# Kernel tuning notes

Hardware: AMD Instinct MI355X
Metric: run time of the kernel (lower is better)

## Reference

```python
import jax, jax.numpy as jnp
import numpy as np

KLD_SCALE = 10.0
COMMIT_COST = 0.25


def setup_inputs() -> dict:
    key = jax.random.key(0)
    k1, k2, k3, k4 = jax.random.split(key, 4)
    B, C, T = 32, 512, 4096
    D, K = 128, 1024
    z = jax.random.normal(k1, (B, C, T), dtype=jnp.float32)
    proj_w = jax.random.normal(k2, (D, C), dtype=jnp.float32) * (1.0 / np.sqrt(C))
    proj_b = jax.random.normal(k3, (D,), dtype=jnp.float32) * 0.01
    embed_w = jax.random.normal(k4, (K, D), dtype=jnp.float32)
    return {"z": z, "proj_w": proj_w, "proj_b": proj_b, "embed_w": embed_w}


def reference(z, proj_w, proj_b, embed_w):
    B, C, T = z.shape
    D = proj_w.shape[0]
    # 1x1 Conv1d == per-timestep linear: [B,C,T] x [D,C] -> [B,T,D]
    z_e = jnp.einsum('bct,dc->btd', z, proj_w) + proj_b
    flat = z_e.reshape(-1, D)  # [B*T, D]
    # squared euclidean distances to codebook: [B*T, K]
    dist = (jnp.sum(flat * flat, axis=1, keepdims=True)
            - 2.0 * (flat @ embed_w.T)
            + jnp.sum(embed_w * embed_w, axis=1)[None, :])
    ind = jnp.argmin(dist, axis=1).reshape(B, T)  # == argmax(-dist)
    z_q = embed_w[ind]  # [B,T,D] codebook gather
    sg = jax.lax.stop_gradient
    diff = KLD_SCALE * (COMMIT_COST * jnp.mean((sg(z_q) - z_e) ** 2)
                        + jnp.mean((z_q - sg(z_e)) ** 2))
    z_q_ste = z_e + sg(z_q - z_e)  # straight-through estimator
    z_q_out = jnp.transpose(z_q_ste, (0, 2, 1))  # [B,D,T]
    return z_q_out, diff, ind
```

## Files before the change

kernel.cpp:

```cpp
#include <hip/hip_runtime.h>

#define B_N 32
#define C_N 512
#define T_N 4096
#define D_N 128
#define K_N 1024
#define N_N (B_N * T_N)

typedef _Float16 f16x8 __attribute__((ext_vector_type(8)));
typedef float    f32x4 __attribute__((ext_vector_type(4)));

#define ZSWZ_OFF 0
#define ESWZ_OFF 67108864
#define ENS_OFF  67895296
#define WSWZ_OFF 68431872
#define PART_OFF 68694016

#define GLL(g, s) __builtin_amdgcn_global_load_lds( \
    (const __attribute__((address_space(1))) unsigned int*)(g), \
    (__attribute__((address_space(3))) unsigned int*)(s), 16, 0, 0)

__global__ __launch_bounds__(128) void k_eprep(const float* __restrict__ E,
                                               _Float16* __restrict__ eswz,
                                               float* __restrict__ ens) {
  __shared__ float s2[2];
  const int code = blockIdx.x, d = threadIdx.x;
  const float e  = E[(size_t)code * D_N + d];
  const float es = e * 64.f;
  const _Float16 eh = (_Float16)es;
  const _Float16 el = (_Float16)(es - (float)eh);

  float sq = es * es;
  #pragma unroll
  for (int off = 32; off > 0; off >>= 1) sq += __shfl_down(sq, off);
  if ((d & 63) == 0) s2[d >> 6] = sq;
  __syncthreads();
  if (d == 0) ens[code] = s2[0] + s2[1];

  const int kt = code >> 7, mi = (code >> 4) & 7, lrow = code & 15;
  const int lk = (d >> 3) & 3, i = d & 7, cb = d >> 5;
  const size_t tile = (size_t)kt * 12;
  #define PUT(c, v) eswz[(((tile + (c)) * 512 + mi * 64 + lk * 16 + lrow) << 3) + i] = (v)
  PUT(cb, eh);
  PUT(4 + cb, el);
  PUT(8 + cb, eh);
  #undef PUT
}

__global__ __launch_bounds__(256) void k_wprep(const float* __restrict__ W,
                                               _Float16* __restrict__ wswz) {
  const int e = blockIdx.x * 256 + threadIdx.x;
  const int d = e >> 9, c = e & 511;
  const float x = W[d * C_N + c] * 8.f;
  const _Float16 h  = (_Float16)x;
  const _Float16 lo = (_Float16)(x - (float)h);
  const int kc = c >> 5, gg = (c >> 3) & 3, j = c & 7;
  const int nf = d >> 4, ll = gg * 16 + (d & 15);
  const size_t base = (size_t)kc * 8192 + ((size_t)nf * 64 + ll) * 8 + j;
  wswz[base]        = h;
  wswz[base + 4096] = lo;
}

__global__ __launch_bounds__(256, 2) void k_projm(const float* __restrict__ z,
                                                  const _Float16* __restrict__ wswz,
                                                  const float* __restrict__ bias,
                                                  f16x8* __restrict__ zswz) {
  __shared__ __align__(16) char lds[65536];

  const int tid = threadIdx.x;
  const int l   = tid & 63, w = tid >> 6;
  const int g   = l >> 4, li = l & 15;
  const int b   = blockIdx.y, t0 = blockIdx.x * 128;
  const float* zb = z + (size_t)b * C_N * T_N + t0;

  float bs[8];
  #pragma unroll
  for (int nf = 0; nf < 8; ++nf) bs[nf] = bias[nf * 16 + li] * 64.f;

  f32x4 acc[2][8];
  #pragma unroll
  for (int mi = 0; mi < 2; ++mi)
    #pragma unroll
    for (int nf = 0; nf < 8; ++nf) acc[mi][nf] = (f32x4)0.f;

  auto stage = [&](int kc, int buf) {
    char* zdst = lds + buf * 16384;
    char* wdst = lds + 32768 + buf * 16384;
    #pragma unroll
    for (int s = 0; s < 4; ++s) {
      const int q = w * 4 + s;
      const unsigned v = q * 64 + l;
      const unsigned u = v ^ (((v >> 8) & 1) << 2);
      GLL((const char*)zb +
              ((size_t)(kc * 32 + (u >> 5)) * T_N + (size_t)(u & 31) * 4) * 4,
          zdst + q * 1024);
      GLL((const char*)wswz + (size_t)kc * 16384 + q * 1024 + l * 16,
          wdst + q * 1024);
    }
  };

  stage(0, 0);
  __syncthreads();

  int buf = 0;
  for (int kc = 0; kc < 16; ++kc) {
    if (kc + 1 < 16) stage(kc + 1, buf ^ 1);

    const float* zl = (const float*)(lds + buf * 16384);
    const f16x8* wb = (const f16x8*)(lds + 32768 + buf * 16384);

    f16x8 ah[2], al[2];
    #pragma unroll
    for (int mi = 0; mi < 2; ++mi) {
      const int mt = w * 2 + mi;
      const int a0 = (g * 1024 + mt * 16 + li) ^ ((g & 1) << 4);
      #pragma unroll
      for (int j = 0; j < 8; ++j) {
        const float x = zl[a0 + j * 128] * 8.f;
        const _Float16 h = (_Float16)x;
        ah[mi][j] = h;
        al[mi][j] = (_Float16)(x - (float)h);
      }
    }
    f16x8 bh[8], bl[8];
    #pragma unroll
    for (int nf = 0; nf < 8; ++nf) {
      bh[nf] = wb[nf * 64 + l];
      bl[nf] = wb[512 + nf * 64 + l];
    }
    #pragma unroll
    for (int mi = 0; mi < 2; ++mi)
      #pragma unroll
      for (int nf = 0; nf < 8; ++nf) {
        acc[mi][nf] = __builtin_amdgcn_mfma_f32_16x16x32_f16(ah[mi], bh[nf], acc[mi][nf], 0, 0, 0);
        acc[mi][nf] = __builtin_amdgcn_mfma_f32_16x16x32_f16(al[mi], bh[nf], acc[mi][nf], 0, 0, 0);
        acc[mi][nf] = __builtin_amdgcn_mfma_f32_16x16x32_f16(ah[mi], bl[nf], acc[mi][nf], 0, 0, 0);
      }
    __syncthreads();
    buf ^= 1;
  }

  unsigned* cs = (unsigned*)lds;
  const int n0 = b * T_N + t0;
  for (int p = 0; p < 2; ++p) {
    #pragma unroll
    for (int mi = 0; mi < 2; ++mi) {
      const int trow = (w * 2 + mi) * 16 + g * 4;
      #pragma unroll
      for (int nfl = 0; nfl < 4; ++nfl) {
        const int nf = p * 4 + nfl;
        #pragma unroll
        for (int r = 0; r < 4; ++r) {
          const float x = acc[mi][nf][r] + bs[nf];
          const _Float16 h  = (_Float16)x;
          const _Float16 lo = (_Float16)(x - (float)h);
          cs[(trow + r) * 68 + nfl * 16 + li] =
              (unsigned)__builtin_bit_cast(unsigned short, h) |
              ((unsigned)__builtin_bit_cast(unsigned short, lo) << 16);
        }
      }
    }
    __syncthreads();
    #pragma unroll
    for (int i = 0; i < 4; ++i) {
      const int u = i * 256 + tid;
      const int t = u & 127, dc = u >> 7;
      f16x8 vh, vl;
      #pragma unroll
      for (int e = 0; e < 8; ++e) {
        const unsigned vv = cs[t * 68 + dc * 8 + e];
        vh[e] = __builtin_bit_cast(_Float16, (unsigned short)(vv & 0xffff));
        vl[e] = __builtin_bit_cast(_Float16, (unsigned short)(vv >> 16));
      }
      const int n = n0 + t;
      const int cu = p * 2 + (dc >> 2), lk = dc & 3;
      const size_t idx = ((size_t)(n >> 4) * 8 + cu) * 64 + lk * 16 + (n & 15);
      zswz[idx]       = vh;
      zswz[idx + 256] = vl;
    }
    __syncthreads();
  }
}

template<int NF0>
__device__ __forceinline__ float gather_lds(int wc, int l, const int* skf,
                                            const float* E, float* ob,
                                            const f16x8* rows) {
  float psum = 0.f;
  #pragma unroll
  for (int nl = 0; nl < 2; ++nl) {
    const int nf = NF0 + nl;
    const int r = wc * 64 + nf * 16 + (l & 15);
    const int k = skf[r];
    const float* Er = E + (size_t)k * D_N;
    #pragma unroll
    for (int cu = 0; cu < 4; ++cu) {
      const int d0 = cu * 32 + (l >> 4) * 8;
      const float4 e0 = *(const float4*)(Er + d0);
      const float4 e1 = *(const float4*)(Er + d0 + 4);
      const float ev[8] = {e0.x, e0.y, e0.z, e0.w, e1.x, e1.y, e1.z, e1.w};
      const f16x8 hi = rows[(((wc * 4 + nf) * 8 + cu) * 64) + l];
      const f16x8 lo = rows[(((wc * 4 + nf) * 8 + cu + 4) * 64) + l];
      #pragma unroll
      for (int j = 0; j < 8; ++j) {
        const float ze = ((float)hi[j] + (float)lo[j]) * 0.015625f;
        const float df = ev[j] - ze;
        psum += df * df;
        ob[(size_t)(d0 + j) * T_N + r] = ev[j];
      }
    }
  }
  return psum;
}

__global__ __launch_bounds__(256, 2) void k_argmin3(const f16x8* __restrict__ zswz,
                                                    const f16x8* __restrict__ eswz,
                                                    const float* __restrict__ ens,
                                                    const float* __restrict__ E,
                                                    float* __restrict__ out,
                                                    float* __restrict__ indf,
                                                    float* __restrict__ part) {
  __shared__ f16x8 rows[4096];
  __shared__ f16x8 abuf[2][512];

  const int tid = threadIdx.x;
  const int l   = tid & 63, w = tid >> 6;
  const int wr  = w >> 1, wc = w & 1;
  const int blk = blockIdx.x;

  const char* zsrc = (const char*)zswz + (size_t)blk * 65536;
  #pragma unroll
  for (int s = 0; s < 16; ++s)
    GLL(zsrc + s * 4096 + tid * 16, &rows[s * 256 + w * 64]);

  {
    const char* asrc = (const char*)eswz;
    GLL(asrc + tid * 16,        &abuf[0][w * 64]);
    GLL(asrc + 4096 + tid * 16, &abuf[0][256 + w * 64]);
  }
  __syncthreads();

  f16x8 bfr[8][4];
  #pragma unroll
  for (int cu = 0; cu < 8; ++cu)
    #pragma unroll
    for (int nf = 0; nf < 4; ++nf)
      bfr[cu][nf] = rows[((wc * 4 + nf) * 8 + cu) * 64 + l];

  float bestd[4];
  int   bestk[4];
  #pragma unroll
  for (int nf = 0; nf < 4; ++nf) { bestd[nf] = 3.4e38f; bestk[nf] = 0; }

  int buf = 0;
  for (int kt = 0; kt < 8; ++kt) {
    f32x4 acc[4][4];
    #pragma unroll
    for (int mi = 0; mi < 4; ++mi)
      #pragma unroll
      for (int nf = 0; nf < 4; ++nf) acc[mi][nf] = (f32x4)0.f;

    #pragma unroll
    for (int c = 0; c < 12; ++c) {
      int nkt = kt, nc = c + 1;
      if (nc == 12) { nc = 0; ++nkt; }
      if (nkt < 8) {
        const char* asrc = (const char*)eswz + ((size_t)(nkt * 12 + nc) * 512) * 16;
        GLL(asrc + tid * 16,        &abuf[buf ^ 1][w * 64]);
        GLL(asrc + 4096 + tid * 16, &abuf[buf ^ 1][256 + w * 64]);
      }
      const int cu = (c < 8) ? (c & 3) : (c - 4);
      f16x8 afr[4];
      #pragma unroll
      for (int mi = 0; mi < 4; ++mi)
        afr[mi] = abuf[buf][(wr * 4 + mi) * 64 + l];
      #pragma unroll
      for (int mi = 0; mi < 4; ++mi)
        #pragma unroll
        for (int nf = 0; nf < 4; ++nf)
          acc[mi][nf] = __builtin_amdgcn_mfma_f32_16x16x32_f16(
              afr[mi], bfr[cu][nf], acc[mi][nf], 0, 0, 0);
      __syncthreads();
      buf ^= 1;
    }

    #pragma unroll
    for (int mi = 0; mi < 4; ++mi) {
      const int cbase = kt * 128 + wr * 64 + mi * 16 + ((l >> 4) << 2);
      const float4 e4 = *(const float4*)&ens[cbase];
      const float ev[4] = {e4.x, e4.y, e4.z, e4.w};
      #pragma unroll
      for (int r = 0; r < 4; ++r) {
        const int k = cbase + r;
        #pragma unroll
        for (int nf = 0; nf < 4; ++nf) {
          const float dv = ev[r] - 2.0f * acc[mi][nf][r];
          if (dv < bestd[nf]) { bestd[nf] = dv; bestk[nf] = k; }
        }
      }
    }
  }

  float* sdl = (float*)abuf;
  int*   skl = (int*)((float*)abuf + 256);
  int*   skf = (int*)((float*)abuf + 512);
  #pragma unroll
  for (int nf = 0; nf < 4; ++nf) {
    float d = bestd[nf]; int k = bestk[nf];
    #pragma unroll
    for (int off = 16; off < 64; off <<= 1) {
      const float od = __shfl_xor(d, off);
      const int   ok = __shfl_xor(k, off);
      if (od < d || (od == d && ok < k)) { d = od; k = ok; }
    }
    if (l < 16) {
      sdl[wr * 128 + wc * 64 + nf * 16 + l] = d;
      skl[wr * 128 + wc * 64 + nf * 16 + l] = k;
    }
  }
  __syncthreads();
  if (tid < 128) {
    float d0 = sdl[tid], d1 = sdl[128 + tid];
    int   k0 = skl[tid], k1 = skl[128 + tid];
    if (d1 < d0 || (d1 == d0 && k1 < k0)) { d0 = d1; k0 = k1; }
    skf[tid] = k0;
    indf[blk * 128 + tid] = (float)k0;
  }
  __syncthreads();

  const int b  = blk >> 5;
  const int t0 = (blk & 31) << 7;
  float* ob = out + (size_t)b * (D_N * T_N) + t0;
  float psum = (wr == 0) ? gather_lds<0>(wc, l, skf, E, ob, rows)
                         : gather_lds<2>(wc, l, skf, E, ob, rows);
  #pragma unroll
  for (int off = 32; off > 0; off >>= 1) psum += __shfl_xor(psum, off);
  if (l == 0) part[blk * 4 + w] = psum;
}

__global__ __launch_bounds__(256) void k_diff(const float* __restrict__ part,
                                              float* __restrict__ diff_out) {
  __shared__ double wsd[4];
  const int tid = threadIdx.x;
  double s = 0.0;
  for (int i = tid; i < 4096; i += 256) s += (double)part[i];
  #pragma unroll
  for (int off = 32; off > 0; off >>= 1) s += __shfl_down(s, off);
  if ((tid & 63) == 0) wsd[tid >> 6] = s;
  __syncthreads();
  if (tid == 0) {
    const double tot = wsd[0] + wsd[1] + wsd[2] + wsd[3];
    diff_out[0] = (float)(12.5 * tot / (double)((size_t)N_N * D_N));
  }
}

extern "C" void kernel_launch(void* const* d_in, const int* in_sizes, int n_in,
                              void* d_out, int out_size, void* d_ws, size_t ws_size,
                              hipStream_t stream) {
  const float* z    = (const float*)d_in[0];
  const float* W    = (const float*)d_in[1];
  const float* bias = (const float*)d_in[2];
  const float* E    = (const float*)d_in[3];

  float* out = (float*)d_out;
  float* out_q    = out;
  float* out_diff = out + 16777216;
  float* out_ind  = out + 16777217;

  char* ws = (char*)d_ws;
  f16x8*    zswz = (f16x8*)(ws + ZSWZ_OFF);
  _Float16* eswz = (_Float16*)(ws + ESWZ_OFF);
  float*    ens  = (float*)(ws + ENS_OFF);
  _Float16* wswz = (_Float16*)(ws + WSWZ_OFF);
  float*    part = (float*)(ws + PART_OFF);

  k_eprep<<<K_N, 128, 0, stream>>>(E, eswz, ens);
  k_wprep<<<256, 256, 0, stream>>>(W, wswz);
  k_projm<<<dim3(T_N / 128, B_N), 256, 0, stream>>>(z, wswz, bias, zswz);
  k_argmin3<<<N_N / 128, 256, 0, stream>>>(zswz, (const f16x8*)eswz, ens, E,
                                           out_q, out_ind, part);
  k_diff<<<1, 256, 0, stream>>>(part, out_diff);
}
```

Baseline: 240.2 us.

## Reuse z staging LDS for larger double-buffered codebook tiles in argmin kernel

The argmin kernel now stages the z tile into a 64KB shared buffer, copies it to registers, then reuses that same buffer as two 32KB codebook stages. Each stage holds four K-chunks, so the kernel syncs once per four MFMA groups instead of once per group. The final gather reads the z_e hi/lo halves from the register fragments instead of LDS. This cuts barrier count and total LDS footprint, at the cost of an explicit vmcnt wait and larger prefetch bursts.

Measured after the change: 214.8 us. 10.6% less time.

```diff
diff --git a/kernel.cpp b/kernel.cpp
--- a/kernel.cpp
+++ b/kernel.cpp
@@ -183,13 +183,14 @@
 }
 
 template<int NF0>
-__device__ __forceinline__ float gather_lds(int wc, int l, const int* skf,
+__device__ __forceinline__ float gather_reg(int wc, int l, const int* skf,
                                             const float* E, float* ob,
-                                            const f16x8* rows) {
+                                            const f16x8 (&bfr)[8][4]) {
   float psum = 0.f;
   #pragma unroll
   for (int nl = 0; nl < 2; ++nl) {
-    const int nf = NF0 + nl;
+    constexpr int NFA[2] = {NF0, NF0 + 1};
+    const int nf = NFA[nl];
     const int r = wc * 64 + nf * 16 + (l & 15);
     const int k = skf[r];
     const float* Er = E + (size_t)k * D_N;
@@ -199,8 +200,8 @@
       const float4 e0 = *(const float4*)(Er + d0);
       const float4 e1 = *(const float4*)(Er + d0 + 4);
       const float ev[8] = {e0.x, e0.y, e0.z, e0.w, e1.x, e1.y, e1.z, e1.w};
-      const f16x8 hi = rows[(((wc * 4 + nf) * 8 + cu) * 64) + l];
-      const f16x8 lo = rows[(((wc * 4 + nf) * 8 + cu + 4) * 64) + l];
+      const f16x8 hi = bfr[cu][nf];
+      const f16x8 lo = bfr[cu + 4][nf];
       #pragma unroll
       for (int j = 0; j < 8; ++j) {
         const float ze = ((float)hi[j] + (float)lo[j]) * 0.015625f;
@@ -213,31 +214,27 @@
   return psum;
 }
 
-__global__ __launch_bounds__(256, 2) void k_argmin3(const f16x8* __restrict__ zswz,
+__global__ __launch_bounds__(256, 2) void k_argmin4(const f16x8* __restrict__ zswz,
                                                     const f16x8* __restrict__ eswz,
                                                     const float* __restrict__ ens,
                                                     const float* __restrict__ E,
                                                     float* __restrict__ out,
                                                     float* __restrict__ indf,
                                                     float* __restrict__ part) {
-  __shared__ f16x8 rows[4096];
-  __shared__ f16x8 abuf[2][512];
-
-  const int tid = threadIdx.x;
-  const int l   = tid & 63, w = tid >> 6;
-  const int wr  = w >> 1, wc = w & 1;
+  __shared__ __align__(16) char sbuf[65536];
+  __shared__ float sdl[256];
+  __shared__ int   skl[256];
+  __shared__ int   skf[128];
+
+  const int tid = threadIdx.x, l = tid & 63, w = tid >> 6;
+  const int wr = w >> 1, wc = w & 1;
   const int blk = blockIdx.x;
 
   const char* zsrc = (const char*)zswz + (size_t)blk * 65536;
   #pragma unroll
   for (int s = 0; s < 16; ++s)
-    GLL(zsrc + s * 4096 + tid * 16, &rows[s * 256 + w * 64]);
-
-  {
-    const char* asrc = (const char*)eswz;
-    GLL(asrc + tid * 16,        &abuf[0][w * 64]);
-    GLL(asrc + 4096 + tid * 16, &abuf[0][256 + w * 64]);
-  }
+    GLL(zsrc + s * 4096 + tid * 16, sbuf + s * 4096 + w * 1024);
+  asm volatile("s_waitcnt vmcnt(0)" ::: "memory");
   __syncthreads();
 
   f16x8 bfr[8][4];
@@ -245,14 +242,22 @@
   for (int cu = 0; cu < 8; ++cu)
     #pragma unroll
     for (int nf = 0; nf < 4; ++nf)
-      bfr[cu][nf] = rows[((wc * 4 + nf) * 8 + cu) * 64 + l];
+      bfr[cu][nf] =
+          *(const f16x8*)(sbuf + (((((wc * 4 + nf) * 8 + cu) * 64) + l) << 4));
+  __syncthreads();
+
+  const char* easrc = (const char*)eswz;
+  #pragma unroll
+  for (int s = 0; s < 4; ++s) {
+    GLL(easrc + s * 8192 + tid * 16,        sbuf + s * 8192 + w * 1024);
+    GLL(easrc + s * 8192 + 4096 + tid * 16, sbuf + s * 8192 + 4096 + w * 1024);
+  }
 
   float bestd[4];
   int   bestk[4];
   #pragma unroll
   for (int nf = 0; nf < 4; ++nf) { bestd[nf] = 3.4e38f; bestk[nf] = 0; }
 
-  int buf = 0;
   for (int kt = 0; kt < 8; ++kt) {
     f32x4 acc[4][4];
     #pragma unroll
@@ -261,27 +266,41 @@
       for (int nf = 0; nf < 4; ++nf) acc[mi][nf] = (f32x4)0.f;
 
     #pragma unroll
-    for (int c = 0; c < 12; ++c) {
-      int nkt = kt, nc = c + 1;
-      if (nc == 12) { nc = 0; ++nkt; }
-      if (nkt < 8) {
-        const char* asrc = (const char*)eswz + ((size_t)(nkt * 12 + nc) * 512) * 16;
-        GLL(asrc + tid * 16,        &abuf[buf ^ 1][w * 64]);
-        GLL(asrc + 4096 + tid * 16, &abuf[buf ^ 1][256 + w * 64]);
-      }
-      const int cu = (c < 8) ? (c & 3) : (c - 4);
-      f16x8 afr[4];
-      #pragma unroll
-      for (int mi = 0; mi < 4; ++mi)
-        afr[mi] = abuf[buf][(wr * 4 + mi) * 64 + l];
-      #pragma unroll
-      for (int mi = 0; mi < 4; ++mi)
-        #pragma unroll
-        for (int nf = 0; nf < 4; ++nf)
-          acc[mi][nf] = __builtin_amdgcn_mfma_f32_16x16x32_f16(
-              afr[mi], bfr[cu][nf], acc[mi][nf], 0, 0, 0);
+    for (int pp = 0; pp < 3; ++pp) {
+      const int p = kt * 3 + pp;
+      char* rbuf = sbuf + (size_t)(p & 1) * 32768;
+      char* wbufp = sbuf + (size_t)((p + 1) & 1) * 32768;
+
       __syncthreads();
-      buf ^= 1;
+
+      if (p + 1 < 24) {
+        const size_t nb = (size_t)(p + 1) * 32768;
+        #pragma unroll
+        for (int s = 0; s < 4; ++s) {
+          GLL(easrc + nb + s * 8192 + tid * 16,
+              wbufp + s * 8192 + w * 1024);
+          GLL(easrc + nb + s * 8192 + 4096 + tid * 16,
+              wbufp + s * 8192 + 4096 + w * 1024);
+        }
+      }
+
+      #pragma unroll
+      for (int j = 0; j < 4; ++j) {
+        constexpr int CUMAP[12] = {0, 1, 2, 3, 0, 1, 2, 3, 4, 5, 6, 7};
+        const int c  = pp * 4 + j;
+        const int cu = CUMAP[c];
+        f16x8 afr[4];
+        #pragma unroll
+        for (int mi = 0; mi < 4; ++mi)
+          afr[mi] = *(const f16x8*)(rbuf + (size_t)j * 8192 +
+                                    (((wr * 4 + mi) * 64 + l) << 4));
+        #pragma unroll
+        for (int mi = 0; mi < 4; ++mi)
+          #pragma unroll
+          for (int nf = 0; nf < 4; ++nf)
+            acc[mi][nf] = __builtin_amdgcn_mfma_f32_16x16x32_f16(
+                afr[mi], bfr[cu][nf], acc[mi][nf], 0, 0, 0);
+      }
     }
 
     #pragma unroll
@@ -301,9 +320,6 @@
     }
   }
 
-  float* sdl = (float*)abuf;
-  int*   skl = (int*)((float*)abuf + 256);
-  int*   skf = (int*)((float*)abuf + 512);
   #pragma unroll
   for (int nf = 0; nf < 4; ++nf) {
     float d = bestd[nf]; int k = bestk[nf];
@@ -331,8 +347,8 @@
   const int b  = blk >> 5;
   const int t0 = (blk & 31) << 7;
   float* ob = out + (size_t)b * (D_N * T_N) + t0;
-  float psum = (wr == 0) ? gather_lds<0>(wc, l, skf, E, ob, rows)
-                         : gather_lds<2>(wc, l, skf, E, ob, rows);
+  float psum = (wr == 0) ? gather_reg<0>(wc, l, skf, E, ob, bfr)
+                         : gather_reg<2>(wc, l, skf, E, ob, bfr);
   #pragma unroll
   for (int off = 32; off > 0; off >>= 1) psum += __shfl_xor(psum, off);
   if (l == 0) part[blk * 4 + w] = psum;
@@ -377,7 +393,7 @@
   k_eprep<<<K_N, 128, 0, stream>>>(E, eswz, ens);
   k_wprep<<<256, 256, 0, stream>>>(W, wswz);
   k_projm<<<dim3(T_N / 128, B_N), 256, 0, stream>>>(z, wswz, bias, zswz);
-  k_argmin3<<<N_N / 128, 256, 0, stream>>>(zswz, (const f16x8*)eswz, ens, E,
+  k_argmin4<<<N_N / 128, 256, 0, stream>>>(zswz, (const f16x8*)eswz, ens, E,
                                            out_q, out_ind, part);
   k_diff<<<1, 256, 0, stream>>>(part, out_diff);
 }
```
